# Performance work log

Hardware: AMD Instinct MI355X
Metric: run time of the kernel (lower is better)

Reference implementation:

```python
import jax, jax.numpy as jnp
import numpy as np

N_NODES = 50000
N_EDGES = 800000
IN_DIM = 128
HID = 128
OUT_DIM = 128
N_LAYERS = 6
NUM_GRAPHS = 128


def setup_inputs() -> dict:
    key = jax.random.key(0)
    ks = jax.random.split(key, 16)
    s = 0.05
    inp = {
        "x": jax.random.normal(ks[0], (N_NODES, IN_DIM), jnp.float32),
        "edge_index": jax.random.randint(ks[1], (2, N_EDGES), 0, N_NODES, jnp.int64 if jax.config.jax_enable_x64 else jnp.int32).astype(jnp.int32),
        "batch": jnp.sort(jax.random.randint(ks[2], (N_NODES,), 0, NUM_GRAPHS).astype(jnp.int32)),
        # pre linear
        "pre_w": jax.random.normal(ks[3], (IN_DIM, HID), jnp.float32) * s,
        "pre_b": jnp.zeros((HID,), jnp.float32),
        # GIN mlp per layer: Linear(H,H) -> ReLU -> Linear(H,H)
        "conv_w1": jax.random.normal(ks[4], (N_LAYERS, HID, HID), jnp.float32) * s,
        "conv_b1": jnp.zeros((N_LAYERS, HID), jnp.float32),
        "conv_w2": jax.random.normal(ks[5], (N_LAYERS, HID, HID), jnp.float32) * s,
        "conv_b2": jnp.zeros((N_LAYERS, HID), jnp.float32),
        # post MLP: Linear(7H, H) -> ReLU -> Linear(H, out)
        "post_w1": jax.random.normal(ks[6], (HID * (N_LAYERS + 1), HID), jnp.float32) * s,
        "post_b1": jnp.zeros((HID,), jnp.float32),
        "post_w2": jax.random.normal(ks[7], (HID, OUT_DIM), jnp.float32) * s,
        "post_b2": jnp.zeros((OUT_DIM,), jnp.float32),
    }
    return inp


def reference(x, edge_index, batch, pre_w, pre_b, conv_w1, conv_b1, conv_w2, conv_b2,
              post_w1, post_b1, post_w2, post_b2):
    src, dst = edge_index[0], edge_index[1]
    # pre linear
    h = x @ pre_w + pre_b  # [N, H]
    emb_list = [h]
    xres = h
    for i in range(N_LAYERS):
        # GINConv (eps=0): agg_j x_j over in-edges, then (1+eps)*x + agg -> MLP
        msg = h[src]  # [E, H] gather
        agg = jax.ops.segment_sum(msg, dst, num_segments=N_NODES)  # scatter-add
        z = h + agg
        z = jax.nn.relu(z @ conv_w1[i] + conv_b1[i]) @ conv_w2[i] + conv_b2[i]
        if i & 1:
            z = z + xres
            xres = z
        h = jax.nn.relu(z)
        emb_list.append(h)
    emb = jnp.concatenate(emb_list, axis=1)  # [N, (L+1)*H]
    # global add pool over graphs
    pooled = jax.ops.segment_sum(emb, batch, num_segments=NUM_GRAPHS)  # [G, (L+1)*H]
    out = jax.nn.relu(pooled @ post_w1 + post_b1) @ post_w2 + post_b2  # [G, OUT]
    return out
```

## Files before the change

kernel.cpp:

```cpp
#include <hip/hip_runtime.h>
#include <hip/hip_bf16.h>

#define HID 128

using bf16x8 = __attribute__((ext_vector_type(8))) short;
using f32x4  = __attribute__((ext_vector_type(4))) float;

__device__ inline float bf2f(unsigned int u16) {
    union { float f; unsigned int i; } v; v.i = u16 << 16; return v.f;
}
__device__ inline unsigned short f2bf(float f) {
    __hip_bfloat16 h = __float2bfloat16(f);
    return *reinterpret_cast<unsigned short*>(&h);
}


__global__ void zero_i32(int* __restrict__ p, int n) {
    int i = blockIdx.x * blockDim.x + threadIdx.x;
    if (i < n) p[i] = 0;
}

__global__ void count_deg(const int* __restrict__ dst, int* __restrict__ deg, int E) {
    int e = blockIdx.x * blockDim.x + threadIdx.x;
    if (e < E) atomicAdd(&deg[dst[e]], 1);
}

__global__ __launch_bounds__(256) void block_sums(const int* __restrict__ deg,
                                                  int* __restrict__ bsum, int n) {
    __shared__ int red[256];
    int t = threadIdx.x;
    int i = blockIdx.x * 256 + t;
    red[t] = (i < n) ? deg[i] : 0;
    __syncthreads();
    for (int off = 128; off > 0; off >>= 1) {
        if (t < off) red[t] += red[t + off];
        __syncthreads();
    }
    if (t == 0) bsum[blockIdx.x] = red[0];
}

__global__ __launch_bounds__(1024) void scan_bsums(const int* __restrict__ bsum,
                                                   int* __restrict__ bstart, int nb) {
    __shared__ int s[1024];
    int t = threadIdx.x;
    s[t] = (t < nb) ? bsum[t] : 0;
    __syncthreads();
    for (int off = 1; off < 1024; off <<= 1) {
        int v = (t >= off) ? s[t - off] : 0;
        __syncthreads();
        s[t] += v;
        __syncthreads();
    }
    if (t < nb) bstart[t] = (t == 0) ? 0 : s[t - 1];
}

__global__ __launch_bounds__(256) void scan_within(const int* __restrict__ deg,
                                                   const int* __restrict__ bstart,
                                                   int* __restrict__ row_ptr,
                                                   int* __restrict__ pos, int n) {
    __shared__ int s[256];
    int b = blockIdx.x, t = threadIdx.x;
    int i = b * 256 + t;
    int v = (i < n) ? deg[i] : 0;
    s[t] = v;
    __syncthreads();
    for (int off = 1; off < 256; off <<= 1) {
        int u = (t >= off) ? s[t - off] : 0;
        __syncthreads();
        s[t] += u;
        __syncthreads();
    }
    if (i < n) {
        int excl = bstart[b] + s[t] - v;
        row_ptr[i] = excl;
        pos[i] = excl;
        if (i == n - 1) row_ptr[n] = bstart[b] + s[t];
    }
}

__global__ void fill_csr(const int* __restrict__ src, const int* __restrict__ dst,
                         int* __restrict__ pos, int* __restrict__ csr_src, int E) {
    int e = blockIdx.x * blockDim.x + threadIdx.x;
    if (e < E) {
        int p = atomicAdd(&pos[dst[e]], 1);
        csr_src[p] = src[e];
    }
}

__global__ void graph_starts(const int* __restrict__ batch, int* __restrict__ gstart,
                             int n, int G) {
    int g = blockIdx.x * blockDim.x + threadIdx.x;
    if (g > G) return;
    int lo = 0, hi = n;
    while (lo < hi) { int m = (lo + hi) >> 1; if (batch[m] < g) lo = m + 1; else hi = m; }
    gstart[g] = lo;
}


__global__ void f32_to_bf16_vec(const float* __restrict__ in,
                                unsigned short* __restrict__ out, int n8) {
    int i = blockIdx.x * blockDim.x + threadIdx.x;
    if (i >= n8) return;
    const float4* in4 = (const float4*)in;
    float4 a = in4[i * 2], b = in4[i * 2 + 1];
    uint4 o;
    o.x = f2bf(a.x) | ((unsigned)f2bf(a.y) << 16);
    o.y = f2bf(a.z) | ((unsigned)f2bf(a.w) << 16);
    o.z = f2bf(b.x) | ((unsigned)f2bf(b.y) << 16);
    o.w = f2bf(b.z) | ((unsigned)f2bf(b.w) << 16);
    ((uint4*)out)[i] = o;
}

__global__ void transpose_kc(const float* __restrict__ W, unsigned short* __restrict__ Wt,
                             int K, int C, int total) {
    int tid = blockIdx.x * blockDim.x + threadIdx.x;
    if (tid >= total) return;
    int kc = K * C;
    int mat = tid / kc;
    int rem = tid - mat * kc;
    int c = rem / K;
    int k = rem - c * K;
    Wt[tid] = f2bf(W[(size_t)mat * kc + (size_t)k * C + c]);
}

template <bool ODD>
__global__ __launch_bounds__(256) void fused_layer(const unsigned short* __restrict__ emb,
                                                   int slice_u4, int row_u4,
                                                   const int* __restrict__ row_ptr,
                                                   const int* __restrict__ csr_src,
                                                   const unsigned short* __restrict__ Wt1,
                                                   const float* __restrict__ b1,
                                                   const unsigned short* __restrict__ Wt2,
                                                   const float* __restrict__ b2,
                                                   unsigned short* __restrict__ xres,
                                                   unsigned short* __restrict__ h_out,
                                                   int out_stride, int N) {
    __shared__ __align__(16) char zt[16 * 256];
    __shared__ __align__(16) char tt[16 * 256];
    int t = threadIdx.x;
    int rowbase = blockIdx.x * 16;

    {
        int nl = t >> 4;
        int sub = (t >> 3) & 1;
        int lane8 = t & 7;
        int node = rowbase + nl;
        const uint4* h4 = (const uint4*)emb;
        float sa0=0,sa1=0,sa2=0,sa3=0,sa4=0,sa5=0,sa6=0,sa7=0;
        float sb0=0,sb1=0,sb2=0,sb3=0,sb4=0,sb5=0,sb6=0,sb7=0;
        if (node < N) {
            if (sub == 0) {
                size_t base = (size_t)node * row_u4 + slice_u4;
                uint4 u0 = h4[base + lane8];
                uint4 u1 = h4[base + lane8 + 8];
                sa0 = bf2f(u0.x & 0xffff); sa1 = bf2f(u0.x >> 16);
                sa2 = bf2f(u0.y & 0xffff); sa3 = bf2f(u0.y >> 16);
                sa4 = bf2f(u0.z & 0xffff); sa5 = bf2f(u0.z >> 16);
                sa6 = bf2f(u0.w & 0xffff); sa7 = bf2f(u0.w >> 16);
                sb0 = bf2f(u1.x & 0xffff); sb1 = bf2f(u1.x >> 16);
                sb2 = bf2f(u1.y & 0xffff); sb3 = bf2f(u1.y >> 16);
                sb4 = bf2f(u1.z & 0xffff); sb5 = bf2f(u1.z >> 16);
                sb6 = bf2f(u1.w & 0xffff); sb7 = bf2f(u1.w >> 16);
            }
            int e0 = row_ptr[node], e1 = row_ptr[node + 1];
            int e = e0 + sub;
            for (; e + 2 < e1; e += 4) {
                int i0 = csr_src[e], i1 = csr_src[e + 2];
                size_t p0 = (size_t)i0 * row_u4 + slice_u4;
                size_t p1 = (size_t)i1 * row_u4 + slice_u4;
                uint4 v0 = h4[p0 + lane8];
                uint4 v1 = h4[p0 + lane8 + 8];
                uint4 w0 = h4[p1 + lane8];
                uint4 w1 = h4[p1 + lane8 + 8];
                sa0 += bf2f(v0.x & 0xffff); sa1 += bf2f(v0.x >> 16);
                sa2 += bf2f(v0.y & 0xffff); sa3 += bf2f(v0.y >> 16);
                sa4 += bf2f(v0.z & 0xffff); sa5 += bf2f(v0.z >> 16);
                sa6 += bf2f(v0.w & 0xffff); sa7 += bf2f(v0.w >> 16);
                sb0 += bf2f(v1.x & 0xffff); sb1 += bf2f(v1.x >> 16);
                sb2 += bf2f(v1.y & 0xffff); sb3 += bf2f(v1.y >> 16);
                sb4 += bf2f(v1.z & 0xffff); sb5 += bf2f(v1.z >> 16);
                sb6 += bf2f(v1.w & 0xffff); sb7 += bf2f(v1.w >> 16);
                sa0 += bf2f(w0.x & 0xffff); sa1 += bf2f(w0.x >> 16);
                sa2 += bf2f(w0.y & 0xffff); sa3 += bf2f(w0.y >> 16);
                sa4 += bf2f(w0.z & 0xffff); sa5 += bf2f(w0.z >> 16);
                sa6 += bf2f(w0.w & 0xffff); sa7 += bf2f(w0.w >> 16);
                sb0 += bf2f(w1.x & 0xffff); sb1 += bf2f(w1.x >> 16);
                sb2 += bf2f(w1.y & 0xffff); sb3 += bf2f(w1.y >> 16);
                sb4 += bf2f(w1.z & 0xffff); sb5 += bf2f(w1.z >> 16);
                sb6 += bf2f(w1.w & 0xffff); sb7 += bf2f(w1.w >> 16);
            }
            if (e < e1) {
                size_t p0 = (size_t)csr_src[e] * row_u4 + slice_u4;
                uint4 v0 = h4[p0 + lane8];
                uint4 v1 = h4[p0 + lane8 + 8];
                sa0 += bf2f(v0.x & 0xffff); sa1 += bf2f(v0.x >> 16);
                sa2 += bf2f(v0.y & 0xffff); sa3 += bf2f(v0.y >> 16);
                sa4 += bf2f(v0.z & 0xffff); sa5 += bf2f(v0.z >> 16);
                sa6 += bf2f(v0.w & 0xffff); sa7 += bf2f(v0.w >> 16);
                sb0 += bf2f(v1.x & 0xffff); sb1 += bf2f(v1.x >> 16);
                sb2 += bf2f(v1.y & 0xffff); sb3 += bf2f(v1.y >> 16);
                sb4 += bf2f(v1.z & 0xffff); sb5 += bf2f(v1.z >> 16);
                sb6 += bf2f(v1.w & 0xffff); sb7 += bf2f(v1.w >> 16);
            }
        }
        sa0 += __shfl_xor(sa0, 8); sa1 += __shfl_xor(sa1, 8);
        sa2 += __shfl_xor(sa2, 8); sa3 += __shfl_xor(sa3, 8);
        sa4 += __shfl_xor(sa4, 8); sa5 += __shfl_xor(sa5, 8);
        sa6 += __shfl_xor(sa6, 8); sa7 += __shfl_xor(sa7, 8);
        sb0 += __shfl_xor(sb0, 8); sb1 += __shfl_xor(sb1, 8);
        sb2 += __shfl_xor(sb2, 8); sb3 += __shfl_xor(sb3, 8);
        sb4 += __shfl_xor(sb4, 8); sb5 += __shfl_xor(sb5, 8);
        sb6 += __shfl_xor(sb6, 8); sb7 += __shfl_xor(sb7, 8);
        uint4 o;
        if (sub == 0) {
            o.x = f2bf(sa0) | ((unsigned)f2bf(sa1) << 16);
            o.y = f2bf(sa2) | ((unsigned)f2bf(sa3) << 16);
            o.z = f2bf(sa4) | ((unsigned)f2bf(sa5) << 16);
            o.w = f2bf(sa6) | ((unsigned)f2bf(sa7) << 16);
        } else {
            o.x = f2bf(sb0) | ((unsigned)f2bf(sb1) << 16);
            o.y = f2bf(sb2) | ((unsigned)f2bf(sb3) << 16);
            o.z = f2bf(sb4) | ((unsigned)f2bf(sb5) << 16);
            o.w = f2bf(sb6) | ((unsigned)f2bf(sb7) << 16);
        }
        int chunk = lane8 + sub * 8;
        *(uint4*)(zt + nl * 256 + ((chunk * 16) ^ ((nl & 7) << 4))) = o;
    }
    __syncthreads();

    int wave = t >> 6, lane = t & 63, l15 = lane & 15, l4 = lane >> 4;
    int colbase = wave * 32;

    f32x4 acc[2];
#pragma unroll
    for (int ct = 0; ct < 2; ct++) acc[ct] = (f32x4){0.f, 0.f, 0.f, 0.f};

#pragma unroll
    for (int kk = 0; kk < 4; kk++) {
        int k0 = kk * 32 + l4 * 8;
        bf16x8 a0 = *(const bf16x8*)(zt + l15 * 256 + ((k0 * 2) ^ ((l15 & 7) << 4)));
#pragma unroll
        for (int ct = 0; ct < 2; ct++) {
            bf16x8 b = *(const bf16x8*)&Wt1[(size_t)(colbase + ct * 16 + l15) * HID + k0];
            acc[ct] = __builtin_amdgcn_mfma_f32_16x16x32_bf16(a0, b, acc[ct], 0, 0, 0);
        }
    }

#pragma unroll
    for (int ct = 0; ct < 2; ct++) {
        int col = colbase + ct * 16 + l15;
        float bc = b1[col];
#pragma unroll
        for (int j = 0; j < 4; j++) {
            int r = l4 * 4 + j;
            float v = fmaxf(acc[ct][j] + bc, 0.f);
            *(unsigned short*)(tt + r * 256 + ((col * 2) ^ ((r & 7) << 4))) = f2bf(v);
        }
    }
    __syncthreads();

#pragma unroll
    for (int ct = 0; ct < 2; ct++) acc[ct] = (f32x4){0.f, 0.f, 0.f, 0.f};
#pragma unroll
    for (int kk = 0; kk < 4; kk++) {
        int k0 = kk * 32 + l4 * 8;
        bf16x8 a0 = *(const bf16x8*)(tt + l15 * 256 + ((k0 * 2) ^ ((l15 & 7) << 4)));
#pragma unroll
        for (int ct = 0; ct < 2; ct++) {
            bf16x8 b = *(const bf16x8*)&Wt2[(size_t)(colbase + ct * 16 + l15) * HID + k0];
            acc[ct] = __builtin_amdgcn_mfma_f32_16x16x32_bf16(a0, b, acc[ct], 0, 0, 0);
        }
    }

#pragma unroll
    for (int ct = 0; ct < 2; ct++) {
        int col = colbase + ct * 16 + l15;
        float bc = b2[col];
#pragma unroll
        for (int j = 0; j < 4; j++) {
            int r = l4 * 4 + j;
            int rg = rowbase + r;
            if (rg < N) {
                float v = acc[ct][j] + bc;
                if (ODD) {
                    v += bf2f(xres[(size_t)rg * HID + col]);
                    xres[(size_t)rg * HID + col] = f2bf(v);
                }
                h_out[(size_t)rg * out_stride + col] = f2bf(fmaxf(v, 0.f));
            }
        }
    }
}

__global__ __launch_bounds__(256) void linear_pre(const unsigned short* __restrict__ in,
                                                  const unsigned short* __restrict__ Wt,
                                                  const float* __restrict__ bias,
                                                  unsigned short* __restrict__ out,
                                                  int out_stride,
                                                  unsigned short* __restrict__ pre_out, int M) {
    int tid = threadIdx.x;
    int wave = tid >> 6, lane = tid & 63;
    int l15 = lane & 15, l4 = lane >> 4;
    int rowbase = blockIdx.x * 64 + wave * 16;
    f32x4 acc[8];
#pragma unroll
    for (int ct = 0; ct < 8; ct++) acc[ct] = (f32x4){0.f, 0.f, 0.f, 0.f};
    int r0 = min(rowbase + l15, M - 1);
#pragma unroll
    for (int kk = 0; kk < 4; kk++) {
        int k0 = kk * 32 + l4 * 8;
        bf16x8 a0 = *(const bf16x8*)&in[(size_t)r0 * HID + k0];
#pragma unroll
        for (int ct = 0; ct < 8; ct++) {
            bf16x8 b = *(const bf16x8*)&Wt[(size_t)(ct * 16 + l15) * HID + k0];
            acc[ct] = __builtin_amdgcn_mfma_f32_16x16x32_bf16(a0, b, acc[ct], 0, 0, 0);
        }
    }
#pragma unroll
    for (int ct = 0; ct < 8; ct++) {
        int col = ct * 16 + l15;
        float bc = bias[col];
#pragma unroll
        for (int j = 0; j < 4; j++) {
            int r = rowbase + l4 * 4 + j;
            if (r < M) {
                float v = acc[ct][j] + bc;
                unsigned short bv = f2bf(v);
                pre_out[(size_t)r * HID + col] = bv;
                out[(size_t)r * out_stride + col] = bv;
            }
        }
    }
}

__global__ __launch_bounds__(128) void pool_all(const unsigned short* __restrict__ emb,
                                                const int* __restrict__ gstart,
                                                float* __restrict__ part, int EMB) {
    int g = blockIdx.x >> 3, sub = blockIdx.x & 7;
    int t = threadIdx.x;
    if (t >= 112) return;
    const uint4* e4 = (const uint4*)emb;
    int row_u4 = EMB / 8;
    int n0 = gstart[g], n1 = gstart[g + 1];
    float s[8] = {0.f, 0.f, 0.f, 0.f, 0.f, 0.f, 0.f, 0.f};
    for (int n = n0 + sub; n < n1; n += 8) {
        uint4 v = e4[(size_t)n * row_u4 + t];
        s[0] += bf2f(v.x & 0xffff); s[1] += bf2f(v.x >> 16);
        s[2] += bf2f(v.y & 0xffff); s[3] += bf2f(v.y >> 16);
        s[4] += bf2f(v.z & 0xffff); s[5] += bf2f(v.z >> 16);
        s[6] += bf2f(v.w & 0xffff); s[7] += bf2f(v.w >> 16);
    }
    float4* p4 = (float4*)&part[(size_t)blockIdx.x * EMB + t * 8];
    p4[0] = (float4){s[0], s[1], s[2], s[3]};
    p4[1] = (float4){s[4], s[5], s[6], s[7]};
}

__global__ __launch_bounds__(128) void pool_fin(const float* __restrict__ part,
                                                unsigned short* __restrict__ pooled,
                                                int EMB) {
    int idx = blockIdx.x * 128 + threadIdx.x;
    int g = idx / EMB, c = idx - g * EMB;
    float s = 0.f;
#pragma unroll
    for (int sub = 0; sub < 8; sub++)
        s += part[(size_t)(g * 8 + sub) * EMB + c];
    pooled[idx] = f2bf(s);
}

__global__ __launch_bounds__(256) void post_mfma(const unsigned short* __restrict__ pooled,
                                                 const unsigned short* __restrict__ w1t,
                                                 const float* __restrict__ b1,
                                                 const unsigned short* __restrict__ w2t,
                                                 const float* __restrict__ b2,
                                                 float* __restrict__ out, int EMB) {
    __shared__ __align__(16) char lds[128 * 256];
    int t = threadIdx.x;
    int wave = t >> 6, lane = t & 63, l15 = lane & 15, l4 = lane >> 4;
    int wrow = wave * 32;
    f32x4 acc[2][8];
#pragma unroll
    for (int rt = 0; rt < 2; rt++)
#pragma unroll
        for (int ct = 0; ct < 8; ct++) acc[rt][ct] = (f32x4){0.f, 0.f, 0.f, 0.f};
    int r0 = wrow + l15, r1 = r0 + 16;
#pragma unroll 4
    for (int kk = 0; kk < EMB / 32; kk++) {
        int k0 = kk * 32 + l4 * 8;
        bf16x8 a0 = *(const bf16x8*)&pooled[(size_t)r0 * EMB + k0];
        bf16x8 a1 = *(const bf16x8*)&pooled[(size_t)r1 * EMB + k0];
#pragma unroll
        for (int ct = 0; ct < 8; ct++) {
            bf16x8 b = *(const bf16x8*)&w1t[(size_t)(ct * 16 + l15) * EMB + k0];
            acc[0][ct] = __builtin_amdgcn_mfma_f32_16x16x32_bf16(a0, b, acc[0][ct], 0, 0, 0);
            acc[1][ct] = __builtin_amdgcn_mfma_f32_16x16x32_bf16(a1, b, acc[1][ct], 0, 0, 0);
        }
    }
#pragma unroll
    for (int ct = 0; ct < 8; ct++) {
        int col = ct * 16 + l15;
        float bc = b1[col];
#pragma unroll
        for (int rt = 0; rt < 2; rt++)
#pragma unroll
            for (int j = 0; j < 4; j++) {
                int r = wrow + rt * 16 + l4 * 4 + j;
                float v = fmaxf(acc[rt][ct][j] + bc, 0.f);
                *(unsigned short*)(lds + r * 256 + ((col * 2) ^ ((r & 7) << 4))) = f2bf(v);
            }
    }
    __syncthreads();
#pragma unroll
    for (int rt = 0; rt < 2; rt++)
#pragma unroll
        for (int ct = 0; ct < 8; ct++) acc[rt][ct] = (f32x4){0.f, 0.f, 0.f, 0.f};
#pragma unroll
    for (int kk = 0; kk < 4; kk++) {
        int k0 = kk * 32 + l4 * 8;
        bf16x8 a0 = *(const bf16x8*)(lds + r0 * 256 + ((k0 * 2) ^ ((r0 & 7) << 4)));
        bf16x8 a1 = *(const bf16x8*)(lds + r1 * 256 + ((k0 * 2) ^ ((r1 & 7) << 4)));
#pragma unroll
        for (int ct = 0; ct < 8; ct++) {
            bf16x8 b = *(const bf16x8*)&w2t[(size_t)(ct * 16 + l15) * HID + k0];
            acc[0][ct] = __builtin_amdgcn_mfma_f32_16x16x32_bf16(a0, b, acc[0][ct], 0, 0, 0);
            acc[1][ct] = __builtin_amdgcn_mfma_f32_16x16x32_bf16(a1, b, acc[1][ct], 0, 0, 0);
        }
    }
#pragma unroll
    for (int ct = 0; ct < 8; ct++) {
        int col = ct * 16 + l15;
        float bc = b2[col];
#pragma unroll
        for (int rt = 0; rt < 2; rt++)
#pragma unroll
            for (int j = 0; j < 4; j++) {
                int r = wrow + rt * 16 + l4 * 4 + j;
                out[(size_t)r * HID + col] = acc[rt][ct][j] + bc;
            }
    }
}


extern "C" void kernel_launch(void* const* d_in, const int* in_sizes, int n_in,
                              void* d_out, int out_size, void* d_ws, size_t ws_size,
                              hipStream_t stream) {
    const float* x       = (const float*)d_in[0];
    const int* edge_index= (const int*)d_in[1];
    const int* batch     = (const int*)d_in[2];
    const float* pre_w   = (const float*)d_in[3];
    const float* pre_b   = (const float*)d_in[4];
    const float* conv_w1 = (const float*)d_in[5];
    const float* conv_b1 = (const float*)d_in[6];
    const float* conv_w2 = (const float*)d_in[7];
    const float* conv_b2 = (const float*)d_in[8];
    const float* post_w1 = (const float*)d_in[9];
    const float* post_b1 = (const float*)d_in[10];
    const float* post_w2 = (const float*)d_in[11];
    const float* post_b2 = (const float*)d_in[12];
    float* outp = (float*)d_out;

    int N = in_sizes[0] / HID;
    int E = in_sizes[1] / 2;
    int L = in_sizes[5] / (HID * HID);
    int G = out_size / HID;
    int EMB = (L + 1) * HID;

    const int* src = edge_index;
    const int* dst = edge_index + E;

    char* w = (char*)d_ws;
    auto alloc = [&](size_t bytes) -> char* {
        char* p = w;
        w += (bytes + 255) & ~(size_t)255;
        return p;
    };
    unsigned short* emb   = (unsigned short*)alloc((size_t)N * EMB * 2);
    unsigned short* x_bf  = (unsigned short*)alloc((size_t)N * HID * 2);
    unsigned short* xres  = (unsigned short*)alloc((size_t)N * HID * 2);
    float* part   = (float*)alloc((size_t)G * 8 * EMB * 4);
    unsigned short* pooled = (unsigned short*)alloc((size_t)G * EMB * 2);
    unsigned short* Wt_pre = (unsigned short*)alloc((size_t)HID * HID * 2);
    unsigned short* Wt_c1  = (unsigned short*)alloc((size_t)L * HID * HID * 2);
    unsigned short* Wt_c2  = (unsigned short*)alloc((size_t)L * HID * HID * 2);
    unsigned short* w1t    = (unsigned short*)alloc((size_t)EMB * HID * 2);
    unsigned short* w2t    = (unsigned short*)alloc((size_t)HID * HID * 2);
    int* deg      = (int*)alloc((size_t)(N + 1) * 4);
    int* row_ptr  = (int*)alloc((size_t)(N + 1) * 4);
    int* pos      = (int*)alloc((size_t)(N + 1) * 4);
    int* bsum     = (int*)alloc((size_t)1024 * 4);
    int* bstart   = (int*)alloc((size_t)1024 * 4);
    int* csr_src  = (int*)alloc((size_t)E * 4);
    int* gstart   = (int*)alloc((size_t)(G + 1) * 4);
    (void)ws_size; (void)n_in;

    int eb = (E + 255) / 256;
    int nb = (N + 255) / 256;

    zero_i32<<<nb, 256, 0, stream>>>(deg, N);
    count_deg<<<eb, 256, 0, stream>>>(dst, deg, E);
    block_sums<<<nb, 256, 0, stream>>>(deg, bsum, N);
    scan_bsums<<<1, 1024, 0, stream>>>(bsum, bstart, nb);
    scan_within<<<nb, 256, 0, stream>>>(deg, bstart, row_ptr, pos, N);
    fill_csr<<<eb, 256, 0, stream>>>(src, dst, pos, csr_src, E);
    graph_starts<<<1, 256, 0, stream>>>(batch, gstart, N, G);

    f32_to_bf16_vec<<<(N * HID / 8 + 255) / 256, 256, 0, stream>>>(x, x_bf, N * HID / 8);
    transpose_kc<<<(HID * HID + 255) / 256, 256, 0, stream>>>(pre_w, Wt_pre, HID, HID, HID * HID);
    transpose_kc<<<(L * HID * HID + 255) / 256, 256, 0, stream>>>(conv_w1, Wt_c1, HID, HID, L * HID * HID);
    transpose_kc<<<(L * HID * HID + 255) / 256, 256, 0, stream>>>(conv_w2, Wt_c2, HID, HID, L * HID * HID);
    transpose_kc<<<(EMB * HID + 255) / 256, 256, 0, stream>>>(post_w1, w1t, EMB, HID, EMB * HID);
    transpose_kc<<<(HID * HID + 255) / 256, 256, 0, stream>>>(post_w2, w2t, HID, HID, HID * HID);

    int gb64 = (N + 63) / 64;
    int gb16 = (N + 15) / 16;

    linear_pre<<<gb64, 256, 0, stream>>>(x_bf, Wt_pre, pre_b, emb, EMB, xres, N);

    for (int i = 0; i < L; i++) {
        unsigned short* slice_out = emb + (size_t)(i + 1) * HID;
        if (i & 1) {
            fused_layer<true><<<gb16, 256, 0, stream>>>(
                emb, i * 16, EMB / 8, row_ptr, csr_src,
                Wt_c1 + (size_t)i * HID * HID, conv_b1 + i * HID,
                Wt_c2 + (size_t)i * HID * HID, conv_b2 + i * HID,
                xres, slice_out, EMB, N);
        } else {
            fused_layer<false><<<gb16, 256, 0, stream>>>(
                emb, i * 16, EMB / 8, row_ptr, csr_src,
                Wt_c1 + (size_t)i * HID * HID, conv_b1 + i * HID,
                Wt_c2 + (size_t)i * HID * HID, conv_b2 + i * HID,
                xres, slice_out, EMB, N);
        }
    }

    pool_all<<<G * 8, 128, 0, stream>>>(emb, gstart, part, EMB);
    pool_fin<<<(G * EMB) / 128, 128, 0, stream>>>(part, pooled, EMB);
    post_mfma<<<1, 256, 0, stream>>>(pooled, w1t, post_b1, w2t, post_b2, outp, EMB);
}
```

Before: 524.5 us.

## Gather neighbors from compact ping-pong hidden buffers and unroll edge loop deeper

Each layer now reads neighbor features from a dense N x 128 bf16 buffer (ping-pong hA/hB) instead of a 128-column slice inside the wide N x 896 embedding matrix. Epilogues write both the compact buffer and the embedding slice. Whole 256-byte rows are then contiguous, which should improve cache-line and L2 locality for the random gathers. The edge loop is also unrolled to four neighbors per iteration for more memory-level parallelism, at the cost of an extra store per layer and more registers.

```diff
diff --git a/kernel.cpp b/kernel.cpp
--- a/kernel.cpp
+++ b/kernel.cpp
@@ -124,8 +124,7 @@
 }
 
 template <bool ODD>
-__global__ __launch_bounds__(256) void fused_layer(const unsigned short* __restrict__ emb,
-                                                   int slice_u4, int row_u4,
+__global__ __launch_bounds__(256) void fused_layer(const unsigned short* __restrict__ hprev,
                                                    const int* __restrict__ row_ptr,
                                                    const int* __restrict__ csr_src,
                                                    const unsigned short* __restrict__ Wt1,
@@ -133,7 +132,8 @@
                                                    const unsigned short* __restrict__ Wt2,
                                                    const float* __restrict__ b2,
                                                    unsigned short* __restrict__ xres,
-                                                   unsigned short* __restrict__ h_out,
+                                                   unsigned short* __restrict__ hnext,
+                                                   unsigned short* __restrict__ emb_slice,
                                                    int out_stride, int N) {
     __shared__ __align__(16) char zt[16 * 256];
     __shared__ __align__(16) char tt[16 * 256];
@@ -145,12 +145,12 @@
         int sub = (t >> 3) & 1;
         int lane8 = t & 7;
         int node = rowbase + nl;
-        const uint4* h4 = (const uint4*)emb;
+        const uint4* h4 = (const uint4*)hprev;
         float sa0=0,sa1=0,sa2=0,sa3=0,sa4=0,sa5=0,sa6=0,sa7=0;
         float sb0=0,sb1=0,sb2=0,sb3=0,sb4=0,sb5=0,sb6=0,sb7=0;
         if (node < N) {
             if (sub == 0) {
-                size_t base = (size_t)node * row_u4 + slice_u4;
+                size_t base = (size_t)node * 16;
                 uint4 u0 = h4[base + lane8];
                 uint4 u1 = h4[base + lane8 + 8];
                 sa0 = bf2f(u0.x & 0xffff); sa1 = bf2f(u0.x >> 16);
@@ -164,44 +164,35 @@
             }
             int e0 = row_ptr[node], e1 = row_ptr[node + 1];
             int e = e0 + sub;
-            for (; e + 2 < e1; e += 4) {
-                int i0 = csr_src[e], i1 = csr_src[e + 2];
-                size_t p0 = (size_t)i0 * row_u4 + slice_u4;
-                size_t p1 = (size_t)i1 * row_u4 + slice_u4;
-                uint4 v0 = h4[p0 + lane8];
-                uint4 v1 = h4[p0 + lane8 + 8];
-                uint4 w0 = h4[p1 + lane8];
-                uint4 w1 = h4[p1 + lane8 + 8];
-                sa0 += bf2f(v0.x & 0xffff); sa1 += bf2f(v0.x >> 16);
-                sa2 += bf2f(v0.y & 0xffff); sa3 += bf2f(v0.y >> 16);
-                sa4 += bf2f(v0.z & 0xffff); sa5 += bf2f(v0.z >> 16);
-                sa6 += bf2f(v0.w & 0xffff); sa7 += bf2f(v0.w >> 16);
-                sb0 += bf2f(v1.x & 0xffff); sb1 += bf2f(v1.x >> 16);
-                sb2 += bf2f(v1.y & 0xffff); sb3 += bf2f(v1.y >> 16);
-                sb4 += bf2f(v1.z & 0xffff); sb5 += bf2f(v1.z >> 16);
-                sb6 += bf2f(v1.w & 0xffff); sb7 += bf2f(v1.w >> 16);
-                sa0 += bf2f(w0.x & 0xffff); sa1 += bf2f(w0.x >> 16);
-                sa2 += bf2f(w0.y & 0xffff); sa3 += bf2f(w0.y >> 16);
-                sa4 += bf2f(w0.z & 0xffff); sa5 += bf2f(w0.z >> 16);
-                sa6 += bf2f(w0.w & 0xffff); sa7 += bf2f(w0.w >> 16);
-                sb0 += bf2f(w1.x & 0xffff); sb1 += bf2f(w1.x >> 16);
-                sb2 += bf2f(w1.y & 0xffff); sb3 += bf2f(w1.y >> 16);
-                sb4 += bf2f(w1.z & 0xffff); sb5 += bf2f(w1.z >> 16);
-                sb6 += bf2f(w1.w & 0xffff); sb7 += bf2f(w1.w >> 16);
-            }
-            if (e < e1) {
-                size_t p0 = (size_t)csr_src[e] * row_u4 + slice_u4;
-                uint4 v0 = h4[p0 + lane8];
-                uint4 v1 = h4[p0 + lane8 + 8];
-                sa0 += bf2f(v0.x & 0xffff); sa1 += bf2f(v0.x >> 16);
-                sa2 += bf2f(v0.y & 0xffff); sa3 += bf2f(v0.y >> 16);
-                sa4 += bf2f(v0.z & 0xffff); sa5 += bf2f(v0.z >> 16);
-                sa6 += bf2f(v0.w & 0xffff); sa7 += bf2f(v0.w >> 16);
-                sb0 += bf2f(v1.x & 0xffff); sb1 += bf2f(v1.x >> 16);
-                sb2 += bf2f(v1.y & 0xffff); sb3 += bf2f(v1.y >> 16);
-                sb4 += bf2f(v1.z & 0xffff); sb5 += bf2f(v1.z >> 16);
-                sb6 += bf2f(v1.w & 0xffff); sb7 += bf2f(v1.w >> 16);
-            }
+#define ACC_ROW(v0, v1)                                                   \
+            sa0 += bf2f(v0.x & 0xffff); sa1 += bf2f(v0.x >> 16);          \
+            sa2 += bf2f(v0.y & 0xffff); sa3 += bf2f(v0.y >> 16);          \
+            sa4 += bf2f(v0.z & 0xffff); sa5 += bf2f(v0.z >> 16);          \
+            sa6 += bf2f(v0.w & 0xffff); sa7 += bf2f(v0.w >> 16);          \
+            sb0 += bf2f(v1.x & 0xffff); sb1 += bf2f(v1.x >> 16);          \
+            sb2 += bf2f(v1.y & 0xffff); sb3 += bf2f(v1.y >> 16);          \
+            sb4 += bf2f(v1.z & 0xffff); sb5 += bf2f(v1.z >> 16);          \
+            sb6 += bf2f(v1.w & 0xffff); sb7 += bf2f(v1.w >> 16);
+            for (; e + 6 < e1; e += 8) {
+                size_t p0 = (size_t)csr_src[e] * 16;
+                size_t p1 = (size_t)csr_src[e + 2] * 16;
+                size_t p2 = (size_t)csr_src[e + 4] * 16;
+                size_t p3 = (size_t)csr_src[e + 6] * 16;
+                uint4 a0 = h4[p0 + lane8], a1 = h4[p0 + lane8 + 8];
+                uint4 c0 = h4[p1 + lane8], c1 = h4[p1 + lane8 + 8];
+                uint4 d0 = h4[p2 + lane8], d1 = h4[p2 + lane8 + 8];
+                uint4 f0 = h4[p3 + lane8], f1 = h4[p3 + lane8 + 8];
+                ACC_ROW(a0, a1)
+                ACC_ROW(c0, c1)
+                ACC_ROW(d0, d1)
+                ACC_ROW(f0, f1)
+            }
+            for (; e < e1; e += 2) {
+                size_t p0 = (size_t)csr_src[e] * 16;
+                uint4 a0 = h4[p0 + lane8], a1 = h4[p0 + lane8 + 8];
+                ACC_ROW(a0, a1)
+            }
+#undef ACC_ROW
         }
         sa0 += __shfl_xor(sa0, 8); sa1 += __shfl_xor(sa1, 8);
         sa2 += __shfl_xor(sa2, 8); sa3 += __shfl_xor(sa3, 8);
@@ -286,7 +277,9 @@
                     v += bf2f(xres[(size_t)rg * HID + col]);
                     xres[(size_t)rg * HID + col] = f2bf(v);
                 }
-                h_out[(size_t)rg * out_stride + col] = f2bf(fmaxf(v, 0.f));
+                unsigned short hv = f2bf(fmaxf(v, 0.f));
+                hnext[(size_t)rg * HID + col] = hv;
+                emb_slice[(size_t)rg * out_stride + col] = hv;
             }
         }
     }
@@ -295,8 +288,9 @@
 __global__ __launch_bounds__(256) void linear_pre(const unsigned short* __restrict__ in,
                                                   const unsigned short* __restrict__ Wt,
                                                   const float* __restrict__ bias,
-                                                  unsigned short* __restrict__ out,
+                                                  unsigned short* __restrict__ emb0,
                                                   int out_stride,
+                                                  unsigned short* __restrict__ hcompact,
                                                   unsigned short* __restrict__ pre_out, int M) {
     int tid = threadIdx.x;
     int wave = tid >> 6, lane = tid & 63;
@@ -327,7 +321,8 @@
                 float v = acc[ct][j] + bc;
                 unsigned short bv = f2bf(v);
                 pre_out[(size_t)r * HID + col] = bv;
-                out[(size_t)r * out_stride + col] = bv;
+                hcompact[(size_t)r * HID + col] = bv;
+                emb0[(size_t)r * out_stride + col] = bv;
             }
         }
     }
@@ -474,6 +469,8 @@
         return p;
     };
     unsigned short* emb   = (unsigned short*)alloc((size_t)N * EMB * 2);
+    unsigned short* hA    = (unsigned short*)alloc((size_t)N * HID * 2);
+    unsigned short* hB    = (unsigned short*)alloc((size_t)N * HID * 2);
     unsigned short* x_bf  = (unsigned short*)alloc((size_t)N * HID * 2);
     unsigned short* xres  = (unsigned short*)alloc((size_t)N * HID * 2);
     float* part   = (float*)alloc((size_t)G * 8 * EMB * 4);
@@ -513,23 +510,26 @@
     int gb64 = (N + 63) / 64;
     int gb16 = (N + 15) / 16;
 
-    linear_pre<<<gb64, 256, 0, stream>>>(x_bf, Wt_pre, pre_b, emb, EMB, xres, N);
-
+    linear_pre<<<gb64, 256, 0, stream>>>(x_bf, Wt_pre, pre_b, emb, EMB, hA, xres, N);
+
+    unsigned short* hcur = hA;
+    unsigned short* hnxt = hB;
     for (int i = 0; i < L; i++) {
         unsigned short* slice_out = emb + (size_t)(i + 1) * HID;
         if (i & 1) {
             fused_layer<true><<<gb16, 256, 0, stream>>>(
-                emb, i * 16, EMB / 8, row_ptr, csr_src,
+                hcur, row_ptr, csr_src,
                 Wt_c1 + (size_t)i * HID * HID, conv_b1 + i * HID,
                 Wt_c2 + (size_t)i * HID * HID, conv_b2 + i * HID,
-                xres, slice_out, EMB, N);
+                xres, hnxt, slice_out, EMB, N);
         } else {
             fused_layer<false><<<gb16, 256, 0, stream>>>(
-                emb, i * 16, EMB / 8, row_ptr, csr_src,
+                hcur, row_ptr, csr_src,
                 Wt_c1 + (size_t)i * HID * HID, conv_b1 + i * HID,
                 Wt_c2 + (size_t)i * HID * HID, conv_b2 + i * HID,
-                xres, slice_out, EMB, N);
-        }
+                xres, hnxt, slice_out, EMB, N);
+        }
+        unsigned short* tmp = hcur; hcur = hnxt; hnxt = tmp;
     }
 
     pool_all<<<G * 8, 128, 0, stream>>>(emb, gstart, part, EMB);
```

Measured after the change: 580.7 us. +10.7%, slower.
